# Kernel tuning notes

Measured on AMD Instinct MI355X. Metric: run time of the kernel, lower is better.

Reference implementation:

```python
import jax, jax.numpy as jnp
import numpy as np

CAMS, HEADS, PTS, LAYERS = 6, 8, 2, 3
D, DH, FFN = 256, 32, 512
VZ, VH, VW = 8, 50, 50
NQ = VZ * VH * VW
IN_C = 768
IMG_H, IMG_W = 256, 704
FH, FW = IMG_H // 32, IMG_W // 32   # 8, 22
L = FH * FW                         # 176 tokens per camera
LVIS = 44                           # visible tokens (mask_ratio=0.75)


def _layer_norm(x, g, b, eps=1e-5):
    m = x.mean(-1, keepdims=True)
    v = x.var(-1, keepdims=True)
    return (x - m) / jnp.sqrt(v + eps) * g + b


def _group_norm(x, g, b, groups=16, eps=1e-5):
    B, C = x.shape[0], x.shape[1]
    xg = x.reshape(B, groups, C // groups, *x.shape[2:])
    m = xg.mean(axis=(2, 3, 4, 5), keepdims=True)
    v = xg.var(axis=(2, 3, 4, 5), keepdims=True)
    xg = (xg - m) / jnp.sqrt(v + eps)
    return xg.reshape(x.shape) * g[None, :, None, None, None] + b[None, :, None, None, None]


def _bilinear(val, loc, Hf, Wf):
    # val: [C, HW, heads, dh]; loc: [C, NQ, heads, P, 2] as (x, y) pixel coords
    x, y = loc[..., 0], loc[..., 1]
    x0 = jnp.floor(x); y0 = jnp.floor(y)
    wx, wy = x - x0, y - y0
    x0i, y0i = x0.astype(jnp.int32), y0.astype(jnp.int32)
    cidx = jnp.arange(val.shape[0])[:, None, None, None]
    hidx = jnp.arange(val.shape[2])[None, None, :, None]

    def g(yi, xi):
        idx = jnp.clip(yi, 0, Hf - 1) * Wf + jnp.clip(xi, 0, Wf - 1)
        return val[cidx, idx, hidx]  # [C,NQ,heads,P,dh]

    out = ((1 - wx) * (1 - wy))[..., None] * g(y0i, x0i)
    out = out + (wx * (1 - wy))[..., None] * g(y0i, x0i + 1)
    out = out + ((1 - wx) * wy)[..., None] * g(y0i + 1, x0i)
    out = out + (wx * wy)[..., None] * g(y0i + 1, x0i + 1)
    return out


def setup_inputs() -> dict:
    key = jax.random.key(0)
    ks = iter(jax.random.split(key, 48))

    def rn(shape, s=0.02):
        return jax.random.normal(next(ks), shape, jnp.float32) * s

    return {
        'camera_x': jax.random.normal(next(ks), (CAMS, LVIS, IN_C), jnp.float32),
        'camera_ids_restore': jax.random.randint(next(ks), (CAMS, L), 0, L),
        'img_h': IMG_H, 'img_w': IMG_W,
        'mask_token': rn((1, 1, IN_C)),
        'vol_emb': rn((NQ, D), 1.0),
        'W_tc': rn((D, IN_C)), 'b_tc': jnp.zeros((D,), jnp.float32),
        'cams_embeds': rn((CAMS, D), 1.0),
        'level_embeds': rn((1, D), 1.0),
        'W_off': rn((LAYERS, D, HEADS * CAMS * PTS * 2)),
        'b_off': rn((LAYERS, HEADS * CAMS * PTS * 2), 2.0),
        'W_att': rn((LAYERS, D, HEADS * CAMS * PTS)),
        'b_att': jnp.zeros((LAYERS, HEADS * CAMS * PTS), jnp.float32),
        'W_val': rn((LAYERS, D, D)), 'b_val': jnp.zeros((LAYERS, D), jnp.float32),
        'W_out': rn((LAYERS, D, D)), 'b_out': jnp.zeros((LAYERS, D), jnp.float32),
        'ln1_g': jnp.ones((LAYERS, D), jnp.float32), 'ln1_b': jnp.zeros((LAYERS, D), jnp.float32),
        'W_ff1': rn((LAYERS, D, FFN)), 'b_ff1': jnp.zeros((LAYERS, FFN), jnp.float32),
        'W_ff2': rn((LAYERS, FFN, D)), 'b_ff2': jnp.zeros((LAYERS, D), jnp.float32),
        'ln2_g': jnp.ones((LAYERS, D), jnp.float32), 'ln2_b': jnp.zeros((LAYERS, D), jnp.float32),
        'deconv_w': rn((D, D, 2, 2, 2)),
        'gn1_g': jnp.ones((D,), jnp.float32), 'gn1_b': jnp.zeros((D,), jnp.float32),
        'conv3_w': rn((192, D, 3, 3, 3)),
        'gn2_g': jnp.ones((192,), jnp.float32), 'gn2_b': jnp.zeros((192,), jnp.float32),
    }


def _forward(camera_x, camera_ids_restore, img_h, img_w, mask_token, vol_emb, W_tc, b_tc,
             cams_embeds, level_embeds, W_off, b_off, W_att, b_att, W_val, b_val, W_out, b_out,
             ln1_g, ln1_b, W_ff1, b_ff1, W_ff2, b_ff2, ln2_g, ln2_b,
             deconv_w, gn1_g, gn1_b, conv3_w, gn2_g, gn2_b):
    N, Lfull = camera_ids_restore.shape
    # 1) MAE unshuffle: append mask tokens, gather back to original order
    mt = jnp.broadcast_to(mask_token, (N, Lfull - camera_x.shape[1], IN_C)).astype(camera_x.dtype)
    full = jnp.concatenate([camera_x, mt], axis=1)                         # [N,L,C]
    full = jnp.take_along_axis(full, camera_ids_restore[:, :, None], axis=1)
    Hf, Wf = img_h // 32, img_w // 32
    cam_x = jnp.transpose(full, (0, 2, 1)).reshape(1, N, IN_C, Hf, Wf)     # [1,6,768,8,22]
    # 2) 1x1 transfer conv + ReLU
    vf = jax.nn.relu(jnp.einsum('bnchw,oc->bnohw', cam_x, W_tc) + b_tc[None, None, :, None, None])
    # 3) flatten spatial + cam/level embeds -> per-camera feature maps [N,HW,D]
    vf = jnp.transpose(vf.reshape(1, N, D, Hf * Wf), (1, 0, 3, 2))          # [N,1,HW,D]
    vf = vf + cams_embeds[:, None, None, :] + level_embeds[None, None, 0:1, :]
    feat = vf[:, 0]                                                         # [N,HW,D]
    # 4) reference points of volume queries (z slow, h, w fast) -> pixel coords
    ww = (jnp.arange(VW, dtype=jnp.float32) + 0.5) / VW
    hh = (jnp.arange(VH, dtype=jnp.float32) + 0.5) / VH
    grid = jnp.stack([jnp.tile(ww, VH), jnp.repeat(hh, VW)], axis=-1)       # [VH*VW,2]
    ref_pix = jnp.tile(grid, (VZ, 1)) * jnp.array([Wf, Hf], jnp.float32) - 0.5  # [NQ,2]
    # 5) deformable cross-attention volume encoder
    q = vol_emb
    for l in range(LAYERS):
        off = (q @ W_off[l] + b_off[l]).reshape(NQ, HEADS, CAMS, PTS, 2)
        att = jax.nn.softmax((q @ W_att[l] + b_att[l]).reshape(NQ, HEADS, CAMS * PTS), axis=-1)
        att = jnp.transpose(att.reshape(NQ, HEADS, CAMS, PTS), (2, 0, 1, 3))      # [C,NQ,H,P]
        val = (feat @ W_val[l] + b_val[l]).reshape(CAMS, Hf * Wf, HEADS, DH)
        loc = jnp.transpose(ref_pix[:, None, None, None, :] + off, (2, 0, 1, 3, 4))  # [C,NQ,H,P,2]
        sampled = _bilinear(val, loc, Hf, Wf)                                     # [C,NQ,H,P,DH]
        agg = jnp.einsum('cnhp,cnhpd->nhd', att, sampled).reshape(NQ, D)
        q = _layer_norm(q + agg @ W_out[l] + b_out[l], ln1_g[l], ln1_b[l])
        q = _layer_norm(q + jax.nn.relu(q @ W_ff1[l] + b_ff1[l]) @ W_ff2[l] + b_ff2[l], ln2_g[l], ln2_b[l])
    # 6) reshape -> [1, D, VW, VH, VZ] (matches .permute(0,4,3,2,1))
    vol = jnp.transpose(q.reshape(1, VZ, VH, VW, D), (0, 4, 3, 2, 1))
    # 7) deblock: deconv3d(k=2,s=2) -> GN16 -> ReLU -> conv3d(k=3,p=1) -> GN16 -> ReLU
    x = jax.lax.conv_transpose(vol, deconv_w, (2, 2, 2), 'VALID',
                               dimension_numbers=('NCDHW', 'OIDHW', 'NCDHW'))
    x = jax.nn.relu(_group_norm(x, gn1_g, gn1_b))
    x = jax.lax.conv_general_dilated(x, conv3_w, (1, 1, 1), [(1, 1)] * 3,
                                     dimension_numbers=('NCDHW', 'OIDHW', 'NCDHW'))
    x = jax.nn.relu(_group_norm(x, gn2_g, gn2_b))
    return x, cam_x


def reference(camera_x, camera_ids_restore, img_h, img_w, mask_token, vol_emb, W_tc, b_tc,
              cams_embeds, level_embeds, W_off, b_off, W_att, b_att, W_val, b_val, W_out, b_out,
              ln1_g, ln1_b, W_ff1, b_ff1, W_ff2, b_ff2, ln2_g, ln2_b,
              deconv_w, gn1_g, gn1_b, conv3_w, gn2_g, gn2_b):
    return _forward(camera_x, camera_ids_restore, img_h, img_w, mask_token, vol_emb, W_tc, b_tc,
                    cams_embeds, level_embeds, W_off, b_off, W_att, b_att, W_val, b_val, W_out, b_out,
                    ln1_g, ln1_b, W_ff1, b_ff1, W_ff2, b_ff2, ln2_g, ln2_b,
                    deconv_w, gn1_g, gn1_b, conv3_w, gn2_g, gn2_b)
```

## Files before the change

kernel.cpp:

```cpp
#include <hip/hip_runtime.h>
#include <stdint.h>

typedef __attribute__((ext_vector_type(8))) short s16x8;
typedef __attribute__((ext_vector_type(4))) float f32x4;

static __device__ __forceinline__ unsigned short f2bf(float f) {
  unsigned u = __float_as_uint(f);
  u += 0x7FFFu + ((u >> 16) & 1u);
  return (unsigned short)(u >> 16);
}
static __device__ __forceinline__ float bf2f(unsigned short h) {
  return __uint_as_float(((unsigned)h) << 16);
}
static __device__ __forceinline__ void sum8(uint4 u, float& a, float& q) {
  unsigned w[4] = {u.x, u.y, u.z, u.w};
#pragma unroll
  for (int i = 0; i < 4; ++i) {
    float v0 = __uint_as_float((w[i] & 0xFFFFu) << 16);
    float v1 = __uint_as_float(w[i] & 0xFFFF0000u);
    a += v0 + v1;
    q += v0 * v0 + v1 * v1;
  }
}

__global__ void k_wt(const float* __restrict__ in, unsigned short* __restrict__ out,
                     int K, int N, int outL, int total) {
  int idx = blockIdx.x * 256 + threadIdx.x;
  if (idx >= total) return;
  int kn = K * N;
  int l = idx / kn, r = idx - l * kn;
  int k = r / N, n = r - k * N;
  out[(size_t)l * outL + (size_t)n * K + k] = f2bf(in[idx]);
}

__global__ void k_wdc(const float* __restrict__ in, unsigned short* __restrict__ out) {
  int idx = blockIdx.x * 256 + threadIdx.x;
  int n = idx >> 8, k = idx & 255;
  out[idx] = f2bf(in[((size_t)(n & 255)) * 2048 + k * 8 + (n >> 8)]);
}

__global__ void k_wc3(const float* __restrict__ W, unsigned short* __restrict__ T) {
  int idx = blockIdx.x * 256 + threadIdx.x;
  int tap = idx / 49152;
  int rem = idx - tap * 49152;
  int oc = rem >> 8, ic = rem & 255;
  int chunk = ic >> 5, kg = (ic >> 3) & 3, j = ic & 7;
  int ocblk = oc >> 4, lo = oc & 15;
  size_t frag = (size_t)(tap * 8 + chunk) * 12 + ocblk;
  T[(frag * 64 + kg * 16 + lo) * 8 + j] = f2bf(W[(oc * 256 + ic) * 27 + tap]);
}

__global__ void k_cvt(const float* __restrict__ in, unsigned short* __restrict__ out, int n) {
  int i = blockIdx.x * 256 + threadIdx.x;
  if (i < n) out[i] = f2bf(in[i]);
}

__global__ void k_restore(const float* __restrict__ cx, const int* __restrict__ ids,
                          const float* __restrict__ mtok, float* __restrict__ out) {
  int idx = blockIdx.x * 256 + threadIdx.x;
  int p = idx % 176;
  int r = idx / 176;
  int ch = r % 768;
  int c = r / 768;
  int id = ids[c * 176 + p];
  out[idx] = (id < 44) ? cx[((size_t)(c * 44 + id)) * 768 + ch] : mtok[ch];
}

__global__ void k_restoreT(const float* __restrict__ cx, const int* __restrict__ ids,
                           const float* __restrict__ mtok, unsigned short* __restrict__ out) {
  int idx = blockIdx.x * 256 + threadIdx.x;
  int ch = idx % 768;
  int row = idx / 768;
  int c = row / 176, p = row - c * 176;
  int id = ids[c * 176 + p];
  float v = (id < 44) ? cx[((size_t)(c * 44 + id)) * 768 + ch] : mtok[ch];
  out[idx] = f2bf(v);
}

__global__ void k_embadd(unsigned short* __restrict__ featb, const float* __restrict__ cemb,
                         const float* __restrict__ lemb) {
  int idx = blockIdx.x * 256 + threadIdx.x;
  int col = idx & 255;
  int c = idx / (176 * 256);
  featb[idx] = f2bf(bf2f(featb[idx]) + cemb[c * 256 + col] + lemb[col]);
}

__global__ __launch_bounds__(256) void k_gemm(
    const unsigned short* __restrict__ A, int M, int lda,
    const unsigned short* __restrict__ Bt, int K, int N,
    const float* __restrict__ bias, const float* __restrict__ bias2, int n1, int relu,
    float* __restrict__ Cf, unsigned short* __restrict__ Cb, int ldc, int mode) {
  __shared__ short sA[128 * 40];
  const int t = threadIdx.x;
  const int l = t & 63, w = t >> 6;
  const int lo = l & 15, kg = l >> 4;
  const int row0 = blockIdx.x * 128, n0 = blockIdx.y * 64;
  const s16x8 bz = {0, 0, 0, 0, 0, 0, 0, 0};
  f32x4 acc[2][4] = {};
  s16x8 bc[4], bn[4];
#pragma unroll
  for (int nb = 0; nb < 4; ++nb) {
    int n = n0 + nb * 16 + lo;
    bc[nb] = (n < N) ? *(const s16x8*)&Bt[(size_t)n * K + kg * 8] : bz;
  }
  const int stR = t >> 1, stH = t & 1;
  for (int kc = 0; kc < K; kc += 32) {
    const bool pf = (kc + 32 < K);
    if (pf) {
#pragma unroll
      for (int nb = 0; nb < 4; ++nb) {
        int n = n0 + nb * 16 + lo;
        bn[nb] = (n < N) ? *(const s16x8*)&Bt[(size_t)n * K + kc + 32 + kg * 8] : bz;
      }
    }
    __syncthreads();
    {
      int r = row0 + stR;
      uint4 v0 = {0u, 0u, 0u, 0u}, v1 = {0u, 0u, 0u, 0u};
      if (r < M) {
        const unsigned short* src = A + (size_t)r * lda + kc + stH * 16;
        v0 = *(const uint4*)src;
        v1 = *(const uint4*)(src + 8);
      }
      *(uint4*)&sA[stR * 40 + stH * 16] = v0;
      *(uint4*)&sA[stR * 40 + stH * 16 + 8] = v1;
    }
    __syncthreads();
    s16x8 a0 = *(const s16x8*)&sA[(w * 32 + lo) * 40 + kg * 8];
    s16x8 a1 = *(const s16x8*)&sA[(w * 32 + 16 + lo) * 40 + kg * 8];
#pragma unroll
    for (int nb = 0; nb < 4; ++nb) {
      acc[0][nb] = __builtin_amdgcn_mfma_f32_16x16x32_bf16(a0, bc[nb], acc[0][nb], 0, 0, 0);
      acc[1][nb] = __builtin_amdgcn_mfma_f32_16x16x32_bf16(a1, bc[nb], acc[1][nb], 0, 0, 0);
    }
    if (pf) {
#pragma unroll
      for (int nb = 0; nb < 4; ++nb) bc[nb] = bn[nb];
    }
  }
#pragma unroll
  for (int m = 0; m < 2; ++m)
#pragma unroll
    for (int nb = 0; nb < 4; ++nb)
#pragma unroll
      for (int r = 0; r < 4; ++r) {
        int row = row0 + w * 32 + m * 16 + (kg << 2) + r;
        int col = n0 + nb * 16 + lo;
        if (row < M && col < N) {
          float v = acc[m][nb][r];
          if (bias) v += (col < n1) ? bias[col] : bias2[col - n1];
          if (relu) v = fmaxf(v, 0.f);
          if (mode == 0) {
            Cf[(size_t)row * ldc + col] = v;
          } else if (mode == 2) {
            Cb[(size_t)row * ldc + col] = f2bf(v);
          } else {
            int tap = col >> 8, oc = col & 255;
            int z = row / 2500, rr = row - z * 2500;
            int hy = rr / 50, wx = rr - hy * 50;
            int t1 = tap >> 2, t2 = (tap >> 1) & 1, t3 = tap & 1;
            int od = 2 * wx + 1 - t1, oh = 2 * hy + 1 - t2, ow = 2 * z + 1 - t3;
            Cb[((size_t)((od * 100 + oh) * 16 + ow)) * 256 + oc] = f2bf(v);
          }
        }
      }
}

__global__ __launch_bounds__(256) void k_sample(const float* __restrict__ oa,
                                                const float* __restrict__ val,
                                                unsigned short* __restrict__ aggb) {
  __shared__ float sl[96], sw[96];
  int t = threadIdx.x;
  int h = t >> 5, d = t & 31;
  const float* vbh0 = val + (size_t)h * 32 + d;
  for (int r = 0; r < 8; ++r) {
    int n = blockIdx.x * 8 + r;
    if (t < 96) sl[t] = oa[(size_t)n * 288 + 192 + t];
    __syncthreads();
    if (t < 96) {
      int hh = t / 12;
      float mx = -1e30f;
#pragma unroll
      for (int j = 0; j < 12; ++j) mx = fmaxf(mx, sl[hh * 12 + j]);
      sw[t] = __expf(sl[t] - mx);
    }
    __syncthreads();
    float ssum = 0.f;
#pragma unroll
    for (int j = 0; j < 12; ++j) ssum += sw[h * 12 + j];
    float inv = 1.f / ssum;
    float xr = ((float)(n % 50) + 0.5f) * (22.0f / 50.0f) - 0.5f;
    float yr = ((float)((n / 50) % 50) + 0.5f) * (8.0f / 50.0f) - 0.5f;
    float acc = 0.f;
    const float* offn = oa + (size_t)n * 288 + h * 24;
#pragma unroll
    for (int c = 0; c < 6; ++c)
#pragma unroll
      for (int p2 = 0; p2 < 2; ++p2) {
        float x = xr + offn[(c * 2 + p2) * 2];
        float y = yr + offn[(c * 2 + p2) * 2 + 1];
        float x0 = floorf(x), y0 = floorf(y);
        float wx = x - x0, wy = y - y0;
        int ix0 = min(max((int)x0, 0), 21), ix1 = min(max((int)x0 + 1, 0), 21);
        int iy0 = min(max((int)y0, 0), 7), iy1 = min(max((int)y0 + 1, 0), 7);
        const float* vb = vbh0 + (size_t)c * 176 * 256;
        float v00 = vb[(size_t)(iy0 * 22 + ix0) * 256];
        float v01 = vb[(size_t)(iy0 * 22 + ix1) * 256];
        float v10 = vb[(size_t)(iy1 * 22 + ix0) * 256];
        float v11 = vb[(size_t)(iy1 * 22 + ix1) * 256];
        float bil = (1.f - wx) * (1.f - wy) * v00 + wx * (1.f - wy) * v01 +
                    (1.f - wx) * wy * v10 + wx * wy * v11;
        acc += sw[h * 12 + c * 2 + p2] * inv * bil;
      }
    aggb[(size_t)n * 256 + t] = f2bf(acc);
    __syncthreads();
  }
}

__global__ __launch_bounds__(256) void k_addln(float* __restrict__ q, const float* __restrict__ p,
                                               const float* __restrict__ g, const float* __restrict__ b,
                                               unsigned short* __restrict__ qb) {
  __shared__ float red[8];
  int t = threadIdx.x;
  int w = t >> 6;
  float gg = g[t], bb = b[t];
  for (int r = 0; r < 8; ++r) {
    size_t n = (size_t)blockIdx.x * 8 + r;
    float x = q[n * 256 + t] + p[n * 256 + t];
    float s1 = x, s2 = x * x;
#pragma unroll
    for (int o = 32; o >= 1; o >>= 1) {
      s1 += __shfl_xor(s1, o, 64);
      s2 += __shfl_xor(s2, o, 64);
    }
    if ((t & 63) == 0) { red[w * 2] = s1; red[w * 2 + 1] = s2; }
    __syncthreads();
    s1 = red[0] + red[2] + red[4] + red[6];
    s2 = red[1] + red[3] + red[5] + red[7];
    float mean = s1 * (1.0f / 256.0f);
    float var = s2 * (1.0f / 256.0f) - mean * mean;
    float y = (x - mean) * rsqrtf(var + 1e-5f) * gg + bb;
    q[n * 256 + t] = y;
    qb[n * 256 + t] = f2bf(y);
    __syncthreads();
  }
}

__global__ __launch_bounds__(256) void k_gnstat1(const unsigned short* __restrict__ X, float* __restrict__ part) {
  __shared__ float s1[256], s2[256];
  int b = blockIdx.x, t = threadIdx.x;
  int oc8 = t & 31, v0 = t >> 5;
  float a = 0.f, q = 0.f;
#pragma unroll
  for (int i = 0; i < 8; ++i) {
    int vox = v0 + i * 8;
    uint4 u = *(const uint4*)&X[(size_t)b * 16384 + vox * 256 + oc8 * 8];
    sum8(u, a, q);
  }
  s1[t] = a; s2[t] = q;
  __syncthreads();
  if (t < 128) { s1[t] += s1[t + 128]; s2[t] += s2[t + 128]; }
  __syncthreads();
  if (t < 64) { s1[t] += s1[t + 64]; s2[t] += s2[t + 64]; }
  __syncthreads();
  if (t < 32) { s1[t] += s1[t + 32]; s2[t] += s2[t + 32]; }
  __syncthreads();
  if (t < 16) {
    part[t * 2500 + b] = s1[2 * t] + s1[2 * t + 1];
    part[40000 + t * 2500 + b] = s2[2 * t] + s2[2 * t + 1];
  }
}

__global__ __launch_bounds__(256) void k_gnred1(const float* __restrict__ part, float* __restrict__ gmv) {
  __shared__ float s1[256], s2[256];
  int g = blockIdx.x, t = threadIdx.x;
  float a = 0.f, q = 0.f;
  for (int i = t; i < 2500; i += 256) { a += part[g * 2500 + i]; q += part[40000 + g * 2500 + i]; }
  s1[t] = a; s2[t] = q;
  __syncthreads();
  for (int s = 128; s > 0; s >>= 1) {
    if (t < s) { s1[t] += s1[t + s]; s2[t] += s2[t + s]; }
    __syncthreads();
  }
  if (t == 0) {
    float m = s1[0] / 2560000.0f;
    float v = s2[0] / 2560000.0f - m * m;
    gmv[2 * g] = m; gmv[2 * g + 1] = rsqrtf(v + 1e-5f);
  }
}

__global__ __launch_bounds__(256) void k_gnapply1(unsigned short* __restrict__ X, const float* __restrict__ gmv,
                                                  const float* __restrict__ g, const float* __restrict__ b) {
  for (unsigned i = blockIdx.x * 256 + threadIdx.x; i < 5120000u; i += gridDim.x * 256) {
    unsigned e = i * 8u;
    int oc0 = e & 255, grp = oc0 >> 4;
    float mean = gmv[grp * 2], rstd = gmv[grp * 2 + 1];
    float4 g0 = *(const float4*)&g[oc0], g1 = *(const float4*)&g[oc0 + 4];
    float4 b0 = *(const float4*)&b[oc0], b1 = *(const float4*)&b[oc0 + 4];
    uint4 u = *(const uint4*)&X[e];
    unsigned w[4] = {u.x, u.y, u.z, u.w};
    float gg[8] = {g0.x, g0.y, g0.z, g0.w, g1.x, g1.y, g1.z, g1.w};
    float bb[8] = {b0.x, b0.y, b0.z, b0.w, b1.x, b1.y, b1.z, b1.w};
    unsigned o[4];
#pragma unroll
    for (int j = 0; j < 4; ++j) {
      float v0 = __uint_as_float((w[j] & 0xFFFFu) << 16);
      float v1 = __uint_as_float(w[j] & 0xFFFF0000u);
      v0 = fmaxf((v0 - mean) * rstd * gg[2 * j] + bb[2 * j], 0.f);
      v1 = fmaxf((v1 - mean) * rstd * gg[2 * j + 1] + bb[2 * j + 1], 0.f);
      o[j] = (unsigned)f2bf(v0) | ((unsigned)f2bf(v1) << 16);
    }
    *(uint4*)&X[e] = make_uint4(o[0], o[1], o[2], o[3]);
  }
}

__global__ __launch_bounds__(256, 2) void k_conv3(const unsigned short* __restrict__ X,
                                                  const unsigned short* __restrict__ Wp,
                                                  unsigned short* __restrict__ Y) {
  __shared__ short sX[4 * 543 * 8];
  int bid = blockIdx.x;
  int xcd = bid & 7, idx = bid >> 3;
  int swz = (xcd < 4 ? xcd * 163 : 652 + (xcd - 4) * 162) + idx;
  const int od = swz / 13;
  const int oh0 = (swz - od * 13) * 8;
  const int t = threadIdx.x;
  const int l = t & 63, w = t >> 6;
  const int kg = l >> 4, lo = l & 15;
  f32x4 acc[8][3] = {};
  s16x8 bc[9], bn[9];
  const unsigned short* Wl = Wp + (size_t)l * 8;
  const int w3 = w * 3;
#pragma unroll
  for (int t2 = 0; t2 < 3; ++t2)
#pragma unroll
    for (int nb = 0; nb < 3; ++nb)
      bc[t2 * 3 + nb] = *(const s16x8*)&Wl[(size_t)((t2 * 3 * 8) * 12 + w3 + nb) * 512];

  for (int gi = 0; gi < 72; ++gi) {
    const int chunk = gi / 9;
    const int sub = gi - chunk * 9;
    const int t1 = sub / 3, t3 = sub - t1 * 3;
    if (sub == 0) {
      __syncthreads();
#pragma unroll
      for (int i = 0; i < 9; ++i) {
        int e = t + i * 256;
        if (e < 2160) {
          int pos = e >> 2, ks = e & 3;
          int sd = pos / 180, r2 = pos - sd * 180;
          int sh = r2 / 18, sw_ = r2 - sh * 18;
          int gd = od + sd - 1, gh = oh0 + sh - 1, gw = sw_ - 1;
          uint4 v = {0u, 0u, 0u, 0u};
          if ((unsigned)gd < 100u && (unsigned)gh < 100u && (unsigned)gw < 16u)
            v = *(const uint4*)&X[((size_t)((gd * 100 + gh) * 16 + gw)) * 256 + chunk * 32 + ks * 8];
          *(uint4*)&sX[(ks * 543 + pos) * 8] = v;
        }
      }
      __syncthreads();
    }
    const int gn1 = gi + 1;
    if (gn1 < 72) {
      const int c1 = gn1 / 9, su1 = gn1 - c1 * 9;
      const int t1n = su1 / 3, t3n = su1 - t1n * 3;
#pragma unroll
      for (int t2 = 0; t2 < 3; ++t2)
#pragma unroll
        for (int nb = 0; nb < 3; ++nb)
          bn[t2 * 3 + nb] = *(const s16x8*)&Wl[
              (size_t)(((t1n * 9 + t2 * 3 + t3n) * 8 + c1) * 12 + w3 + nb) * 512];
    }
    const int abase = kg * 543 + t1 * 180 + lo + t3;
#pragma unroll
    for (int sh = 0; sh < 10; ++sh) {
      s16x8 a = *(const s16x8*)&sX[(abase + sh * 18) * 8];
#pragma unroll
      for (int t2 = 0; t2 < 3; ++t2) {
        const int m = sh - t2;
        if (m >= 0 && m < 8) {
          acc[m][0] = __builtin_amdgcn_mfma_f32_16x16x32_bf16(a, bc[t2 * 3 + 0], acc[m][0], 0, 0, 0);
          acc[m][1] = __builtin_amdgcn_mfma_f32_16x16x32_bf16(a, bc[t2 * 3 + 1], acc[m][1], 0, 0, 0);
          acc[m][2] = __builtin_amdgcn_mfma_f32_16x16x32_bf16(a, bc[t2 * 3 + 2], acc[m][2], 0, 0, 0);
        }
      }
    }
#pragma unroll
    for (int i = 0; i < 9; ++i) bc[i] = bn[i];
  }
#pragma unroll
  for (int m = 0; m < 8; ++m) {
    int oh = oh0 + m;
    if (oh < 100) {
#pragma unroll
      for (int nb = 0; nb < 3; ++nb)
#pragma unroll
        for (int r = 0; r < 4; ++r) {
          int oc = w * 48 + nb * 16 + lo;
          int ow = (kg << 2) + r;
          Y[(size_t)oc * 160000 + (size_t)((od * 100 + oh) * 16) + ow] = f2bf(acc[m][nb][r]);
        }
    }
  }
}

__global__ __launch_bounds__(256) void k_gnstat2(const unsigned short* __restrict__ X, float* __restrict__ part) {
  __shared__ float s1[256], s2[256];
  int b = blockIdx.x, t = threadIdx.x;
  int ch = b / 10, pp = b - ch * 10;
  const unsigned short* base = X + (size_t)ch * 160000 + (size_t)pp * 16000;
  float a = 0.f, q = 0.f;
  for (int i = t; i < 2000; i += 256) {
    uint4 u = *(const uint4*)&base[i * 8];
    sum8(u, a, q);
  }
  s1[t] = a; s2[t] = q;
  __syncthreads();
  for (int s = 128; s > 0; s >>= 1) {
    if (t < s) { s1[t] += s1[t + s]; s2[t] += s2[t + s]; }
    __syncthreads();
  }
  if (t == 0) { part[80000 + ch * 10 + pp] = s1[0]; part[81920 + ch * 10 + pp] = s2[0]; }
}

__global__ __launch_bounds__(256) void k_gnred2(const float* __restrict__ part, float* __restrict__ gmv) {
  __shared__ float s1[256], s2[256];
  int g = blockIdx.x, t = threadIdx.x;
  float a = (t < 120) ? part[80000 + g * 120 + t] : 0.f;
  float q = (t < 120) ? part[81920 + g * 120 + t] : 0.f;
  s1[t] = a; s2[t] = q;
  __syncthreads();
  for (int s = 128; s > 0; s >>= 1) {
    if (t < s) { s1[t] += s1[t + s]; s2[t] += s2[t + s]; }
    __syncthreads();
  }
  if (t == 0) {
    float m = s1[0] / 1920000.0f;
    float v = s2[0] / 1920000.0f - m * m;
    gmv[2 * g] = m; gmv[2 * g + 1] = rsqrtf(v + 1e-5f);
  }
}

__global__ __launch_bounds__(256) void k_gnapply2(const unsigned short* __restrict__ X, const float* __restrict__ gmv,
                                                  const float* __restrict__ g, const float* __restrict__ b,
                                                  float* __restrict__ out) {
  for (unsigned i = blockIdx.x * 256 + threadIdx.x; i < 3840000u; i += gridDim.x * 256) {
    unsigned oc = i / 20000u;
    unsigned grp = oc / 12u;
    float mean = gmv[grp * 2], rstd = gmv[grp * 2 + 1];
    float gam = g[oc], bet = b[oc];
    unsigned e = i * 8u;
    uint4 u = *(const uint4*)&X[e];
    unsigned wv[4] = {u.x, u.y, u.z, u.w};
    float o[8];
#pragma unroll
    for (int j = 0; j < 4; ++j) {
      float v0 = __uint_as_float((wv[j] & 0xFFFFu) << 16);
      float v1 = __uint_as_float(wv[j] & 0xFFFF0000u);
      o[2 * j] = fmaxf((v0 - mean) * rstd * gam + bet, 0.f);
      o[2 * j + 1] = fmaxf((v1 - mean) * rstd * gam + bet, 0.f);
    }
    *(float4*)&out[e] = make_float4(o[0], o[1], o[2], o[3]);
    *(float4*)&out[e + 4] = make_float4(o[4], o[5], o[6], o[7]);
  }
}

static inline dim3 gemm_grid(int M, int N) { return dim3((M + 127) / 128, (N + 63) / 64); }

extern "C" void kernel_launch(void* const* d_in, const int* in_sizes, int n_in,
                              void* d_out, int out_size, void* d_ws, size_t ws_size,
                              hipStream_t stream) {
  const float* camera_x = (const float*)d_in[0];
  const int* ids = (const int*)d_in[1];
  const float* mask_tok = (const float*)d_in[4];
  const float* vol_emb = (const float*)d_in[5];
  const float* W_tc = (const float*)d_in[6];
  const float* b_tc = (const float*)d_in[7];
  const float* cams_emb = (const float*)d_in[8];
  const float* lvl_emb = (const float*)d_in[9];
  const float* W_off = (const float*)d_in[10];
  const float* b_off = (const float*)d_in[11];
  const float* W_att = (const float*)d_in[12];
  const float* b_att = (const float*)d_in[13];
  const float* W_val = (const float*)d_in[14];
  const float* b_val = (const float*)d_in[15];
  const float* W_out = (const float*)d_in[16];
  const float* b_out = (const float*)d_in[17];
  const float* ln1_g = (const float*)d_in[18];
  const float* ln1_b = (const float*)d_in[19];
  const float* W_ff1 = (const float*)d_in[20];
  const float* b_ff1 = (const float*)d_in[21];
  const float* W_ff2 = (const float*)d_in[22];
  const float* b_ff2 = (const float*)d_in[23];
  const float* ln2_g = (const float*)d_in[24];
  const float* ln2_b = (const float*)d_in[25];
  const float* deconv_w = (const float*)d_in[26];
  const float* gn1_g = (const float*)d_in[27];
  const float* gn1_b = (const float*)d_in[28];
  const float* conv3_w = (const float*)d_in[29];
  const float* gn2_g = (const float*)d_in[30];
  const float* gn2_b = (const float*)d_in[31];

  char* ws = (char*)d_ws;
  float* q             = (float*)(ws + 0);
  unsigned short* qb   = (unsigned short*)(ws + 20480000);
  float* proj          = (float*)(ws + 30720000);
  float* oa            = (float*)(ws + 51200000);
  unsigned short* aggb = (unsigned short*)(ws + 74240000);
  unsigned short* ffhb = (unsigned short*)(ws + 84480000);
  float* val           = (float*)(ws + 104960000);
  unsigned short* featb= (unsigned short*)(ws + 106041344);
  unsigned short* x1bf = (unsigned short*)(ws + 30720000);
  unsigned short* c3   = (unsigned short*)(ws + 112640000);
  unsigned short* Wt_val = (unsigned short*)(ws + 174080000);
  unsigned short* Wt_oa  = (unsigned short*)(ws + 174473216);
  unsigned short* Wt_out = (unsigned short*)(ws + 174915584);
  unsigned short* Wt_ff1 = (unsigned short*)(ws + 175308800);
  unsigned short* Wt_ff2 = (unsigned short*)(ws + 176095232);
  unsigned short* Wt_dc  = (unsigned short*)(ws + 176881664);
  unsigned short* wc3    = (unsigned short*)(ws + 177930240);
  float* part = (float*)(ws + 180584448);
  float* gmv1 = (float*)(ws + 180920320);
  float* gmv2 = (float*)(ws + 180920448);
  unsigned short* Wt_tc  = (unsigned short*)(ws + 180920576);
  unsigned short* camxT  = (unsigned short*)(ws + 181707008);

  float* out_x = (float*)d_out;
  float* out_camx = out_x + 30720000;

  k_cvt<<<768, 256, 0, stream>>>(W_tc, Wt_tc, 196608);
  k_wt<<<(3 * 65536 + 255) / 256, 256, 0, stream>>>(W_val, Wt_val, 256, 256, 65536, 3 * 65536);
  k_wt<<<(3 * 49152 + 255) / 256, 256, 0, stream>>>(W_off, Wt_oa, 256, 192, 73728, 3 * 49152);
  k_wt<<<(3 * 24576 + 255) / 256, 256, 0, stream>>>(W_att, Wt_oa + 192 * 256, 256, 96, 73728, 3 * 24576);
  k_wt<<<(3 * 65536 + 255) / 256, 256, 0, stream>>>(W_out, Wt_out, 256, 256, 65536, 3 * 65536);
  k_wt<<<(3 * 131072 + 255) / 256, 256, 0, stream>>>(W_ff1, Wt_ff1, 256, 512, 131072, 3 * 131072);
  k_wt<<<(3 * 131072 + 255) / 256, 256, 0, stream>>>(W_ff2, Wt_ff2, 512, 256, 131072, 3 * 131072);
  k_wdc<<<2048, 256, 0, stream>>>(deconv_w, Wt_dc);
  k_wc3<<<5184, 256, 0, stream>>>(conv3_w, wc3);

  k_restore<<<3168, 256, 0, stream>>>(camera_x, ids, mask_tok, out_camx);
  k_restoreT<<<3168, 256, 0, stream>>>(camera_x, ids, mask_tok, camxT);
  k_gemm<<<gemm_grid(1056, 256), 256, 0, stream>>>(camxT, 1056, 768, Wt_tc, 768, 256,
                                                   b_tc, nullptr, 256, 1, nullptr, featb, 256, 2);
  k_embadd<<<1056, 256, 0, stream>>>(featb, cams_emb, lvl_emb);

  hipMemcpyAsync(q, vol_emb, (size_t)20000 * 256 * 4, hipMemcpyDeviceToDevice, stream);
  k_cvt<<<20000, 256, 0, stream>>>(vol_emb, qb, 5120000);

  for (int lyr = 0; lyr < 3; ++lyr) {
    k_gemm<<<gemm_grid(1056, 256), 256, 0, stream>>>(featb, 1056, 256, Wt_val + lyr * 65536, 256, 256,
                                                     b_val + lyr * 256, nullptr, 256, 0, val, nullptr, 256, 0);
    k_gemm<<<gemm_grid(20000, 288), 256, 0, stream>>>(qb, 20000, 256, Wt_oa + lyr * 73728, 256, 288,
                                                      b_off + lyr * 192, b_att + lyr * 96, 192, 0,
                                                      oa, nullptr, 288, 0);
    k_sample<<<2500, 256, 0, stream>>>(oa, val, aggb);
    k_gemm<<<gemm_grid(20000, 256), 256, 0, stream>>>(aggb, 20000, 256, Wt_out + lyr * 65536, 256, 256,
                                                      b_out + lyr * 256, nullptr, 256, 0, proj, nullptr, 256, 0);
    k_addln<<<2500, 256, 0, stream>>>(q, proj, ln1_g + lyr * 256, ln1_b + lyr * 256, qb);
    k_gemm<<<gemm_grid(20000, 512), 256, 0, stream>>>(qb, 20000, 256, Wt_ff1 + lyr * 131072, 256, 512,
                                                      b_ff1 + lyr * 512, nullptr, 512, 1, nullptr, ffhb, 512, 2);
    k_gemm<<<gemm_grid(20000, 256), 256, 0, stream>>>(ffhb, 20000, 512, Wt_ff2 + lyr * 131072, 512, 256,
                                                      b_ff2 + lyr * 256, nullptr, 256, 0, proj, nullptr, 256, 0);
    k_addln<<<2500, 256, 0, stream>>>(q, proj, ln2_g + lyr * 256, ln2_b + lyr * 256, qb);
  }

  k_gemm<<<gemm_grid(20000, 2048), 256, 0, stream>>>(qb, 20000, 256, Wt_dc, 256, 2048,
                                                     nullptr, nullptr, 2048, 0, nullptr, x1bf, 256, 1);

  k_gnstat1<<<2500, 256, 0, stream>>>(x1bf, part);
  k_gnred1<<<16, 256, 0, stream>>>(part, gmv1);
  k_gnapply1<<<2048, 256, 0, stream>>>(x1bf, gmv1, gn1_g, gn1_b);

  k_conv3<<<1300, 256, 0, stream>>>(x1bf, wc3, c3);

  k_gnstat2<<<1920, 256, 0, stream>>>(c3, part);
  k_gnred2<<<16, 256, 0, stream>>>(part, gmv2);
  k_gnapply2<<<2048, 256, 0, stream>>>(c3, gmv2, gn2_g, gn2_b, out_x);
}
```

Baseline: 1.449 ms.

## Fuse weight prep, restore and embedding kernels; batch value GEMM; add LDS-resident deconv kernel

Several changes land together. The nine weight-conversion launches merge into one k_prep kernel, and the two camera restore kernels merge into one. The camera/level embedding add moves into the token-projection GEMM epilogue through a templated MODE. The three per-layer value projections become a single N=768 GEMM done before the loop. The deconv GEMM becomes a dedicated kernel that keeps a 128x256 A tile in swizzled LDS and loops over all 32 output column tiles. These cut launch count and redundant passes over memory. The risk is the deconv: it now runs on only 157 workgroups, which may leave many CUs idle and limit write bandwidth on the large scatter output.

```diff
diff --git a/kernel.cpp b/kernel.cpp
--- a/kernel.cpp
+++ b/kernel.cpp
@@ -23,31 +23,70 @@
   }
 }
 
-__global__ void k_wt(const float* __restrict__ in, unsigned short* __restrict__ out,
-                     int K, int N, int outL, int total) {
+__global__ void k_prep(const float* __restrict__ W_tc, const float* __restrict__ W_val,
+                       const float* __restrict__ W_off, const float* __restrict__ W_att,
+                       const float* __restrict__ W_out, const float* __restrict__ W_ff1,
+                       const float* __restrict__ W_ff2, const float* __restrict__ deconv_w,
+                       const float* __restrict__ conv3_w,
+                       unsigned short* __restrict__ Wt_tc, unsigned short* __restrict__ Wt_val,
+                       unsigned short* __restrict__ Wt_oa, unsigned short* __restrict__ Wt_out,
+                       unsigned short* __restrict__ Wt_ff1, unsigned short* __restrict__ Wt_ff2,
+                       unsigned short* __restrict__ Wt_dc, unsigned short* __restrict__ wc3) {
   int idx = blockIdx.x * 256 + threadIdx.x;
-  if (idx >= total) return;
-  int kn = K * N;
-  int l = idx / kn, r = idx - l * kn;
-  int k = r / N, n = r - k * N;
-  out[(size_t)l * outL + (size_t)n * K + k] = f2bf(in[idx]);
-}
-
-__global__ void k_wdc(const float* __restrict__ in, unsigned short* __restrict__ out) {
-  int idx = blockIdx.x * 256 + threadIdx.x;
-  int n = idx >> 8, k = idx & 255;
-  out[idx] = f2bf(in[((size_t)(n & 255)) * 2048 + k * 8 + (n >> 8)]);
-}
-
-__global__ void k_wc3(const float* __restrict__ W, unsigned short* __restrict__ T) {
-  int idx = blockIdx.x * 256 + threadIdx.x;
-  int tap = idx / 49152;
-  int rem = idx - tap * 49152;
-  int oc = rem >> 8, ic = rem & 255;
-  int chunk = ic >> 5, kg = (ic >> 3) & 3, j = ic & 7;
-  int ocblk = oc >> 4, lo = oc & 15;
-  size_t frag = (size_t)(tap * 8 + chunk) * 12 + ocblk;
-  T[(frag * 64 + kg * 16 + lo) * 8 + j] = f2bf(W[(oc * 256 + ic) * 27 + tap]);
+  if (idx < 196608) { Wt_tc[idx] = f2bf(W_tc[idx]); return; }
+  idx -= 196608;
+  if (idx < 196608) {
+    int l = idx / 65536, r = idx - l * 65536, k = r >> 8, n = r & 255;
+    Wt_val[l * 65536 + n * 256 + k] = f2bf(W_val[l * 65536 + r]);
+    return;
+  }
+  idx -= 196608;
+  if (idx < 147456) {
+    int l = idx / 49152, r = idx - l * 49152, k = r / 192, n = r - k * 192;
+    Wt_oa[l * 73728 + n * 256 + k] = f2bf(W_off[l * 49152 + r]);
+    return;
+  }
+  idx -= 147456;
+  if (idx < 73728) {
+    int l = idx / 24576, r = idx - l * 24576, k = r / 96, n = r - k * 96;
+    Wt_oa[l * 73728 + 192 * 256 + n * 256 + k] = f2bf(W_att[l * 24576 + r]);
+    return;
+  }
+  idx -= 73728;
+  if (idx < 196608) {
+    int l = idx / 65536, r = idx - l * 65536, k = r >> 8, n = r & 255;
+    Wt_out[l * 65536 + n * 256 + k] = f2bf(W_out[l * 65536 + r]);
+    return;
+  }
+  idx -= 196608;
+  if (idx < 393216) {
+    int l = idx / 131072, r = idx - l * 131072, k = r >> 9, n = r & 511;
+    Wt_ff1[l * 131072 + n * 256 + k] = f2bf(W_ff1[l * 131072 + r]);
+    return;
+  }
+  idx -= 393216;
+  if (idx < 393216) {
+    int l = idx / 131072, r = idx - l * 131072, k = r >> 8, n = r & 255;
+    Wt_ff2[l * 131072 + n * 512 + k] = f2bf(W_ff2[l * 131072 + r]);
+    return;
+  }
+  idx -= 393216;
+  if (idx < 524288) {
+    int n = idx >> 8, k = idx & 255;
+    Wt_dc[idx] = f2bf(deconv_w[(size_t)(n & 255) * 2048 + k * 8 + (n >> 8)]);
+    return;
+  }
+  idx -= 524288;
+  if (idx < 1327104) {
+    int tap = idx / 49152;
+    int rem = idx - tap * 49152;
+    int oc = rem >> 8, ic = rem & 255;
+    int chunk = ic >> 5, kg = (ic >> 3) & 3, j = ic & 7;
+    int ocblk = oc >> 4, lo = oc & 15;
+    size_t frag = (size_t)(tap * 8 + chunk) * 12 + ocblk;
+    wc3[(frag * 64 + kg * 16 + lo) * 8 + j] = f2bf(conv3_w[(oc * 256 + ic) * 27 + tap]);
+    return;
+  }
 }
 
 __global__ void k_cvt(const float* __restrict__ in, unsigned short* __restrict__ out, int n) {
@@ -55,41 +94,27 @@
   if (i < n) out[i] = f2bf(in[i]);
 }
 
-__global__ void k_restore(const float* __restrict__ cx, const int* __restrict__ ids,
-                          const float* __restrict__ mtok, float* __restrict__ out) {
+__global__ void k_restore2(const float* __restrict__ cx, const int* __restrict__ ids,
+                           const float* __restrict__ mtok, float* __restrict__ out_camx,
+                           unsigned short* __restrict__ camxT) {
   int idx = blockIdx.x * 256 + threadIdx.x;
-  int p = idx % 176;
-  int r = idx / 176;
-  int ch = r % 768;
-  int c = r / 768;
-  int id = ids[c * 176 + p];
-  out[idx] = (id < 44) ? cx[((size_t)(c * 44 + id)) * 768 + ch] : mtok[ch];
-}
-
-__global__ void k_restoreT(const float* __restrict__ cx, const int* __restrict__ ids,
-                           const float* __restrict__ mtok, unsigned short* __restrict__ out) {
-  int idx = blockIdx.x * 256 + threadIdx.x;
+  if (idx >= 811008) return;
   int ch = idx % 768;
   int row = idx / 768;
   int c = row / 176, p = row - c * 176;
   int id = ids[c * 176 + p];
   float v = (id < 44) ? cx[((size_t)(c * 44 + id)) * 768 + ch] : mtok[ch];
-  out[idx] = f2bf(v);
-}
-
-__global__ void k_embadd(unsigned short* __restrict__ featb, const float* __restrict__ cemb,
-                         const float* __restrict__ lemb) {
-  int idx = blockIdx.x * 256 + threadIdx.x;
-  int col = idx & 255;
-  int c = idx / (176 * 256);
-  featb[idx] = f2bf(bf2f(featb[idx]) + cemb[c * 256 + col] + lemb[col]);
-}
-
+  camxT[idx] = f2bf(v);
+  out_camx[((size_t)(c * 768 + ch)) * 176 + p] = v;
+}
+
+template <int MODE>
 __global__ __launch_bounds__(256) void k_gemm(
     const unsigned short* __restrict__ A, int M, int lda,
     const unsigned short* __restrict__ Bt, int K, int N,
     const float* __restrict__ bias, const float* __restrict__ bias2, int n1, int relu,
-    float* __restrict__ Cf, unsigned short* __restrict__ Cb, int ldc, int mode) {
+    float* __restrict__ Cf, unsigned short* __restrict__ Cb, int ldc,
+    const float* __restrict__ cemb, const float* __restrict__ lemb) {
   __shared__ short sA[128 * 40];
   const int t = threadIdx.x;
   const int l = t & 63, w = t >> 6;
@@ -150,20 +175,83 @@
           float v = acc[m][nb][r];
           if (bias) v += (col < n1) ? bias[col] : bias2[col - n1];
           if (relu) v = fmaxf(v, 0.f);
-          if (mode == 0) {
+          if (MODE == 0) {
             Cf[(size_t)row * ldc + col] = v;
-          } else if (mode == 2) {
+          } else if (MODE == 2) {
             Cb[(size_t)row * ldc + col] = f2bf(v);
           } else {
-            int tap = col >> 8, oc = col & 255;
+            v += cemb[(row / 176) * 256 + col] + lemb[col];
+            Cb[(size_t)row * ldc + col] = f2bf(v);
+          }
+        }
+      }
+}
+
+__global__ __launch_bounds__(256, 2) void k_deconv(const unsigned short* __restrict__ A,
+                                                   const unsigned short* __restrict__ Bt,
+                                                   unsigned short* __restrict__ Cb, int M) {
+  __shared__ short sA[128 * 256];
+  const int t = threadIdx.x;
+  const int l = t & 63, w = t >> 6;
+  const int lo = l & 15, kg = l >> 4;
+  const int row0 = blockIdx.x * 128;
+#pragma unroll
+  for (int i = 0; i < 16; ++i) {
+    int g = t + i * 256;
+    int row = g >> 5, gcol = g & 31;
+    int r = row0 + row;
+    uint4 v = {0u, 0u, 0u, 0u};
+    if (r < M) v = *(const uint4*)&A[(size_t)r * 256 + gcol * 8];
+    *(uint4*)&sA[row * 256 + ((gcol ^ (row & 7)) << 3)] = v;
+  }
+  __syncthreads();
+  const int r0 = w * 32 + lo, r1 = r0 + 16;
+  for (int nt = 0; nt < 32; ++nt) {
+    f32x4 acc[2][4] = {};
+    s16x8 bc[4], bn[4];
+    const int ncol0 = nt * 64;
+#pragma unroll
+    for (int nb = 0; nb < 4; ++nb)
+      bc[nb] = *(const s16x8*)&Bt[(size_t)(ncol0 + nb * 16 + lo) * 256 + kg * 8];
+#pragma unroll
+    for (int kc = 0; kc < 8; ++kc) {
+      const bool pf = kc < 7;
+      if (pf) {
+#pragma unroll
+        for (int nb = 0; nb < 4; ++nb)
+          bn[nb] = *(const s16x8*)&Bt[(size_t)(ncol0 + nb * 16 + lo) * 256 + (kc + 1) * 32 + kg * 8];
+      }
+      int g0 = kc * 4 + kg;
+      s16x8 a0 = *(const s16x8*)&sA[r0 * 256 + ((g0 ^ (r0 & 7)) << 3)];
+      s16x8 a1 = *(const s16x8*)&sA[r1 * 256 + ((g0 ^ (r1 & 7)) << 3)];
+#pragma unroll
+      for (int nb = 0; nb < 4; ++nb) {
+        acc[0][nb] = __builtin_amdgcn_mfma_f32_16x16x32_bf16(a0, bc[nb], acc[0][nb], 0, 0, 0);
+        acc[1][nb] = __builtin_amdgcn_mfma_f32_16x16x32_bf16(a1, bc[nb], acc[1][nb], 0, 0, 0);
+      }
+      if (pf) {
+#pragma unroll
+        for (int nb = 0; nb < 4; ++nb) bc[nb] = bn[nb];
+      }
+    }
+    const int tap = nt >> 2;
+    const int t1 = tap >> 2, t2 = (tap >> 1) & 1, t3 = tap & 1;
+#pragma unroll
+    for (int m = 0; m < 2; ++m)
+#pragma unroll
+      for (int nb = 0; nb < 4; ++nb)
+#pragma unroll
+        for (int r = 0; r < 4; ++r) {
+          int row = row0 + w * 32 + m * 16 + (kg << 2) + r;
+          if (row < M) {
+            int oc = (nt & 3) * 64 + nb * 16 + lo;
             int z = row / 2500, rr = row - z * 2500;
             int hy = rr / 50, wx = rr - hy * 50;
-            int t1 = tap >> 2, t2 = (tap >> 1) & 1, t3 = tap & 1;
             int od = 2 * wx + 1 - t1, oh = 2 * hy + 1 - t2, ow = 2 * z + 1 - t3;
-            Cb[((size_t)((od * 100 + oh) * 16 + ow)) * 256 + oc] = f2bf(v);
+            Cb[((size_t)((od * 100 + oh) * 16 + ow)) * 256 + oc] = f2bf(acc[m][nb][r]);
           }
         }
-      }
+  }
 }
 
 __global__ __launch_bounds__(256) void k_sample(const float* __restrict__ oa,
@@ -203,11 +291,11 @@
         float wx = x - x0, wy = y - y0;
         int ix0 = min(max((int)x0, 0), 21), ix1 = min(max((int)x0 + 1, 0), 21);
         int iy0 = min(max((int)y0, 0), 7), iy1 = min(max((int)y0 + 1, 0), 7);
-        const float* vb = vbh0 + (size_t)c * 176 * 256;
-        float v00 = vb[(size_t)(iy0 * 22 + ix0) * 256];
-        float v01 = vb[(size_t)(iy0 * 22 + ix1) * 256];
-        float v10 = vb[(size_t)(iy1 * 22 + ix0) * 256];
-        float v11 = vb[(size_t)(iy1 * 22 + ix1) * 256];
+        const float* vb = vbh0 + (size_t)c * 176 * 768;
+        float v00 = vb[(size_t)(iy0 * 22 + ix0) * 768];
+        float v01 = vb[(size_t)(iy0 * 22 + ix1) * 768];
+        float v10 = vb[(size_t)(iy1 * 22 + ix0) * 768];
+        float v11 = vb[(size_t)(iy1 * 22 + ix1) * 768];
         float bil = (1.f - wx) * (1.f - wy) * v00 + wx * (1.f - wy) * v01 +
                     (1.f - wx) * wy * v10 + wx * wy * v11;
         acc += sw[h * 12 + c * 2 + p2] * inv * bil;
@@ -506,8 +594,8 @@
   float* oa            = (float*)(ws + 51200000);
   unsigned short* aggb = (unsigned short*)(ws + 74240000);
   unsigned short* ffhb = (unsigned short*)(ws + 84480000);
-  float* val           = (float*)(ws + 104960000);
-  unsigned short* featb= (unsigned short*)(ws + 106041344);
+  float* val3          = (float*)(ws + 104960000);
+  unsigned short* featb= (unsigned short*)(ws + 108204032);
   unsigned short* x1bf = (unsigned short*)(ws + 30720000);
   unsigned short* c3   = (unsigned short*)(ws + 112640000);
   unsigned short* Wt_val = (unsigned short*)(ws + 174080000);
@@ -526,44 +614,40 @@
   float* out_x = (float*)d_out;
   float* out_camx = out_x + 30720000;
 
-  k_cvt<<<768, 256, 0, stream>>>(W_tc, Wt_tc, 196608);
-  k_wt<<<(3 * 65536 + 255) / 256, 256, 0, stream>>>(W_val, Wt_val, 256, 256, 65536, 3 * 65536);
-  k_wt<<<(3 * 49152 + 255) / 256, 256, 0, stream>>>(W_off, Wt_oa, 256, 192, 73728, 3 * 49152);
-  k_wt<<<(3 * 24576 + 255) / 256, 256, 0, stream>>>(W_att, Wt_oa + 192 * 256, 256, 96, 73728, 3 * 24576);
-  k_wt<<<(3 * 65536 + 255) / 256, 256, 0, stream>>>(W_out, Wt_out, 256, 256, 65536, 3 * 65536);
-  k_wt<<<(3 * 131072 + 255) / 256, 256, 0, stream>>>(W_ff1, Wt_ff1, 256, 512, 131072, 3 * 131072);
-  k_wt<<<(3 * 131072 + 255) / 256, 256, 0, stream>>>(W_ff2, Wt_ff2, 512, 256, 131072, 3 * 131072);
-  k_wdc<<<2048, 256, 0, stream>>>(deconv_w, Wt_dc);
-  k_wc3<<<5184, 256, 0, stream>>>(conv3_w, wc3);
-
-  k_restore<<<3168, 256, 0, stream>>>(camera_x, ids, mask_tok, out_camx);
-  k_restoreT<<<3168, 256, 0, stream>>>(camera_x, ids, mask_tok, camxT);
-  k_gemm<<<gemm_grid(1056, 256), 256, 0, stream>>>(camxT, 1056, 768, Wt_tc, 768, 256,
-                                                   b_tc, nullptr, 256, 1, nullptr, featb, 256, 2);
-  k_embadd<<<1056, 256, 0, stream>>>(featb, cams_emb, lvl_emb);
-
+  k_prep<<<13472, 256, 0, stream>>>(W_tc, W_val, W_off, W_att, W_out, W_ff1, W_ff2,
+                                    deconv_w, conv3_w,
+                                    Wt_tc, Wt_val, Wt_oa, Wt_out, Wt_ff1, Wt_ff2, Wt_dc, wc3);
+
+  k_restore2<<<3168, 256, 0, stream>>>(camera_x, ids, mask_tok, out_camx, camxT);
+  k_gemm<4><<<gemm_grid(1056, 256), 256, 0, stream>>>(camxT, 1056, 768, Wt_tc, 768, 256,
+                                                      b_tc, nullptr, 256, 1, nullptr, featb, 256,
+                                                      cams_emb, lvl_emb);
   hipMemcpyAsync(q, vol_emb, (size_t)20000 * 256 * 4, hipMemcpyDeviceToDevice, stream);
   k_cvt<<<20000, 256, 0, stream>>>(vol_emb, qb, 5120000);
 
+  k_gemm<0><<<gemm_grid(1056, 768), 256, 0, stream>>>(featb, 1056, 256, Wt_val, 256, 768,
+                                                      b_val, nullptr, 768, 0, val3, nullptr, 768,
+                                                      nullptr, nullptr);
+
   for (int lyr = 0; lyr < 3; ++lyr) {
-    k_gemm<<<gemm_grid(1056, 256), 256, 0, stream>>>(featb, 1056, 256, Wt_val + lyr * 65536, 256, 256,
-                                                     b_val + lyr * 256, nullptr, 256, 0, val, nullptr, 256, 0);
-    k_gemm<<<gemm_grid(20000, 288), 256, 0, stream>>>(qb, 20000, 256, Wt_oa + lyr * 73728, 256, 288,
-                                                      b_off + lyr * 192, b_att + lyr * 96, 192, 0,
-                                                      oa, nullptr, 288, 0);
-    k_sample<<<2500, 256, 0, stream>>>(oa, val, aggb);
-    k_gemm<<<gemm_grid(20000, 256), 256, 0, stream>>>(aggb, 20000, 256, Wt_out + lyr * 65536, 256, 256,
-                                                      b_out + lyr * 256, nullptr, 256, 0, proj, nullptr, 256, 0);
+    k_gemm<0><<<gemm_grid(20000, 288), 256, 0, stream>>>(qb, 20000, 256, Wt_oa + lyr * 73728, 256, 288,
+                                                         b_off + lyr * 192, b_att + lyr * 96, 192, 0,
+                                                         oa, nullptr, 288, nullptr, nullptr);
+    k_sample<<<2500, 256, 0, stream>>>(oa, val3 + lyr * 256, aggb);
+    k_gemm<0><<<gemm_grid(20000, 256), 256, 0, stream>>>(aggb, 20000, 256, Wt_out + lyr * 65536, 256, 256,
+                                                         b_out + lyr * 256, nullptr, 256, 0,
+                                                         proj, nullptr, 256, nullptr, nullptr);
     k_addln<<<2500, 256, 0, stream>>>(q, proj, ln1_g + lyr * 256, ln1_b + lyr * 256, qb);
-    k_gemm<<<gemm_grid(20000, 512), 256, 0, stream>>>(qb, 20000, 256, Wt_ff1 + lyr * 131072, 256, 512,
-                                                      b_ff1 + lyr * 512, nullptr, 512, 1, nullptr, ffhb, 512, 2);
-    k_gemm<<<gemm_grid(20000, 256), 256, 0, stream>>>(ffhb, 20000, 512, Wt_ff2 + lyr * 131072, 512, 256,
-                                                      b_ff2 + lyr * 256, nullptr, 256, 0, proj, nullptr, 256, 0);
+    k_gemm<2><<<gemm_grid(20000, 512), 256, 0, stream>>>(qb, 20000, 256, Wt_ff1 + lyr * 131072, 256, 512,
+                                                         b_ff1 + lyr * 512, nullptr, 512, 1,
+                                                         nullptr, ffhb, 512, nullptr, nullptr);
+    k_gemm<0><<<gemm_grid(20000, 256), 256, 0, stream>>>(ffhb, 20000, 512, Wt_ff2 + lyr * 131072, 512, 256,
+                                                         b_ff2 + lyr * 256, nullptr, 256, 0,
+                                                         proj, nullptr, 256, nullptr, nullptr);
     k_addln<<<2500, 256, 0, stream>>>(q, proj, ln2_g + lyr * 256, ln2_b + lyr * 256, qb);
   }
 
-  k_gemm<<<gemm_grid(20000, 2048), 256, 0, stream>>>(qb, 20000, 256, Wt_dc, 256, 2048,
-                                                     nullptr, nullptr, 2048, 0, nullptr, x1bf, 256, 1);
+  k_deconv<<<157, 256, 0, stream>>>(qb, Wt_dc, x1bf, 20000);
 
   k_gnstat1<<<2500, 256, 0, stream>>>(x1bf, part);
   k_gnred1<<<16, 256, 0, stream>>>(part, gmv1);
```

Measured after the change: 1.431 ms. No clear change (-1.2%).
